# Kernel tuning notes

Measured on AMD Instinct MI355X. Metric: run time of the kernel, lower is better.

## Reference

```python
import jax, jax.numpy as jnp
import numpy as np

B, N, E = 8, 10000, 160000
D_IN, D_H = 128, 128
EPS = 1e-5


def setup_inputs() -> dict:
    key = jax.random.key(0)
    ks = jax.random.split(key, 10)
    x = jax.random.normal(ks[0], (B, N, D_IN), dtype=jnp.float32)
    h_prev = jax.random.normal(ks[1], (B, N, D_H), dtype=jnp.float32)
    edge_index = jax.random.randint(ks[2], (2, E), 0, N, dtype=jnp.int32)
    d_cat = D_IN + D_H
    s = 1.0 / np.sqrt(d_cat)
    def w(k):
        return jax.random.uniform(k, (d_cat, D_H), jnp.float32, -s, s)
    def b(k):
        return jax.random.uniform(k, (D_H,), jnp.float32, -s, s)
    return {
        "x": x, "edge_index": edge_index, "h_prev": h_prev,
        "Wz": w(ks[3]), "bz": b(ks[4]),
        "Wr": w(ks[5]), "br": b(ks[6]),
        "Wc": w(ks[7]), "bc": b(ks[8]),
        "gamma": jnp.ones((D_H,), jnp.float32),
        "beta": jnp.zeros((D_H,), jnp.float32),
    }


def _gcn(x, W, bias, src, dst, norm, n_nodes):
    # PyG GCNConv: linear transform, gather from src, weight by sym-norm, scatter-add to dst
    msg = (x @ W)[src] * norm[:, None]          # [E_total, D_H]
    return jax.ops.segment_sum(msg, dst, num_segments=n_nodes) + bias


def reference(x, edge_index, h_prev, Wz, bz, Wr, br, Wc, bc, gamma, beta):
    Bx, Nx, _ = x.shape
    BN = Bx * Nx
    x_flat = x.reshape(BN, -1)
    h_flat = h_prev.reshape(BN, -1)

    # batch the edge index with per-graph node offsets (all edges are in-range)
    offsets = (jnp.arange(Bx, dtype=edge_index.dtype) * Nx)[:, None]
    src = (edge_index[0][None, :] + offsets).reshape(-1)
    dst = (edge_index[1][None, :] + offsets).reshape(-1)

    # GCN self-loops + symmetric normalization (shared by all three convs)
    loops = jnp.arange(BN, dtype=src.dtype)
    src = jnp.concatenate([src, loops])
    dst = jnp.concatenate([dst, loops])
    deg = jax.ops.segment_sum(jnp.ones_like(dst, dtype=x.dtype), dst, num_segments=BN)
    dis = jnp.where(deg > 0, 1.0 / jnp.sqrt(jnp.maximum(deg, 1.0)), 0.0)
    norm = dis[src] * dis[dst]

    xh = jnp.concatenate([x_flat, h_flat], axis=1)
    z = jax.nn.sigmoid(_gcn(xh, Wz, bz, src, dst, norm, BN))
    r = jax.nn.sigmoid(_gcn(xh, Wr, br, src, dst, norm, BN))
    xrh = jnp.concatenate([x_flat, r * h_flat], axis=1)
    h_cand = jnp.tanh(_gcn(xrh, Wc, bc, src, dst, norm, BN))

    h_new = (1.0 - z) * h_flat + z * h_cand

    # LayerNorm over last dim
    mu = h_new.mean(axis=-1, keepdims=True)
    var = ((h_new - mu) ** 2).mean(axis=-1, keepdims=True)
    h_new = (h_new - mu) / jnp.sqrt(var + EPS) * gamma + beta
    return h_new.reshape(Bx, Nx, -1)
```

## Files before the change

kernel.cpp:

```cpp
#include <hip/hip_runtime.h>

#define NN 10000
#define BB 8
#define EE 160000
#define DH 128
#define LN_EPS 1e-5f

typedef unsigned short ushort_t;
typedef unsigned int uint_t;

typedef __bf16 bf16x8 __attribute__((ext_vector_type(8)));
typedef float floatx4 __attribute__((ext_vector_type(4)));
typedef float floatx2 __attribute__((ext_vector_type(2)));

__device__ __forceinline__ float b2f(uint_t u) { return __uint_as_float(u << 16); }
__device__ __forceinline__ ushort_t f2b(float f) {
    uint_t u = __float_as_uint(f);
    return (ushort_t)((u + 0x7fffu + ((u >> 16) & 1u)) >> 16);
}
__device__ __forceinline__ uint_t pack2(float lo, float hi) {
    return (uint_t)f2b(lo) | ((uint_t)f2b(hi) << 16);
}
__device__ __forceinline__ float sigm(float x) { return 1.0f / (1.0f + __expf(-x)); }
__device__ __forceinline__ float tanh_fast(float x) {
    float ex = __expf(2.0f * x);
    return 1.0f - 2.0f / (ex + 1.0f);
}

__device__ __forceinline__ floatx2 unpk(uint_t u) {
    floatx2 r;
    r.x = __uint_as_float(u << 16);
    r.y = __uint_as_float(u & 0xffff0000u);
    return r;
}
__device__ __forceinline__ void pk_fma(floatx2& a, floatx2 w, floatx2 v) {
    asm("v_pk_fma_f32 %0, %1, %2, %0" : "+v"(a) : "v"(w), "v"(v));
}
__device__ __forceinline__ void acc8p(floatx2* a, floatx2 w2, uint4 v) {
    pk_fma(a[0], w2, unpk(v.x));
    pk_fma(a[1], w2, unpk(v.y));
    pk_fma(a[2], w2, unpk(v.z));
    pk_fma(a[3], w2, unpk(v.w));
}


__global__ void count_deg(const int* __restrict__ ei, int* __restrict__ cnt) {
    int e = blockIdx.x * 256 + threadIdx.x;
    if (e < EE) atomicAdd(&cnt[ei[EE + e]], 1);
}

__global__ __launch_bounds__(256) void scan1(const int* __restrict__ cnt,
                                             int* __restrict__ offs,
                                             int* __restrict__ bsum) {
    __shared__ int s[256];
    const int t = threadIdx.x, idx = blockIdx.x * 256 + t;
    int x = (idx < NN) ? cnt[idx] : 0;
    s[t] = x;
    __syncthreads();
    for (int o = 1; o < 256; o <<= 1) {
        int v = s[t];
        int u = (t >= o) ? s[t - o] : 0;
        __syncthreads();
        s[t] = v + u;
        __syncthreads();
    }
    if (idx < NN) offs[idx] = s[t] - x;
    if (t == 255) bsum[blockIdx.x] = s[255];
}

__global__ __launch_bounds__(256) void scan3(const int* __restrict__ cnt,
                                             const int* __restrict__ bsum,
                                             int* __restrict__ offs,
                                             int* __restrict__ cursor,
                                             float* __restrict__ dis) {
    __shared__ int sb[40];
    __shared__ int pfx;
    const int t = threadIdx.x;
    if (t < 40) sb[t] = bsum[t];
    __syncthreads();
    if (t == 0) {
        int a = 0;
        for (int i = 0; i < blockIdx.x; ++i) a += sb[i];
        pfx = a;
    }
    __syncthreads();
    const int idx = blockIdx.x * 256 + t;
    if (idx < NN) {
        int off = offs[idx] + pfx;
        offs[idx] = off;
        cursor[idx] = off;
        dis[idx] = rsqrtf((float)(cnt[idx] + 1));
    }
    if (idx == 0) offs[NN] = EE;
}

__global__ void fill_csr(const int* __restrict__ ei, int* __restrict__ cursor,
                         const float* __restrict__ dis, int* __restrict__ csr_src,
                         ushort_t* __restrict__ csr_w) {
    int e = blockIdx.x * 256 + threadIdx.x;
    if (e < EE) {
        int s = ei[e];
        int d = ei[EE + e];
        int pos = atomicAdd(&cursor[d], 1);
        csr_src[pos] = s;
        csr_w[pos] = f2b(dis[s]);
    }
}


__global__ __launch_bounds__(256) void packwt_k(const float* __restrict__ x,
                                                const float* __restrict__ h,
                                                ushort_t* __restrict__ xb,
                                                ushort_t* __restrict__ hb,
                                                const float* __restrict__ Wz,
                                                const float* __restrict__ Wr,
                                                const float* __restrict__ Wc,
                                                ushort_t* __restrict__ Wt_zr,
                                                ushort_t* __restrict__ Wt_c) {
    if (blockIdx.x < 10000) {
        const size_t o = ((size_t)blockIdx.x * 256 + threadIdx.x) * 4;
        float4 vx = *(const float4*)(x + o);
        uint2 px;
        px.x = pack2(vx.x, vx.y);
        px.y = pack2(vx.z, vx.w);
        *(uint2*)(xb + o) = px;
        float4 vh = *(const float4*)(h + o);
        uint2 ph;
        ph.x = pack2(vh.x, vh.y);
        ph.y = pack2(vh.z, vh.w);
        *(uint2*)(hb + o) = ph;
    } else {
        const int col = blockIdx.x - 10000, k = threadIdx.x;
        if (col < 256) {
            float v = (col < 128) ? Wz[(size_t)k * 128 + col]
                                  : Wr[(size_t)k * 128 + col - 128];
            Wt_zr[(size_t)col * 256 + k] = f2b(v);
        } else {
            int c2 = col - 256;
            Wt_c[(size_t)c2 * 256 + k] = f2b(Wc[(size_t)k * 128 + c2]);
        }
    }
}


template <int NB>
__global__ __launch_bounds__(256) void gather4(
    const ushort_t* __restrict__ src0, const ushort_t* __restrict__ src1,
    const int* __restrict__ offs, const int* __restrict__ csr_src,
    const ushort_t* __restrict__ csr_w, const float* __restrict__ dis,
    ushort_t* __restrict__ dst0, ushort_t* __restrict__ dst1) {
    const int tid = threadIdx.x, lane = tid & 63;
    const int b = blockIdx.x & 7;
    const int n = (blockIdx.x >> 3) * 4 + (tid >> 6);
    const int g = lane >> 4, il = lane & 15;
    const ushort_t* base0 = src0 + (size_t)b * NN * 128;
    const ushort_t* base1 = (NB == 2) ? (src1 + (size_t)b * NN * 128) : base0;

    floatx2 a0[4], a1[4];
#pragma unroll
    for (int j = 0; j < 4; ++j) {
        a0[j] = (floatx2){0.f, 0.f};
        a1[j] = (floatx2){0.f, 0.f};
    }

    const float dn = dis[n];
    if (g == 0) {
        const floatx2 d2 = {dn, dn};
        const uint_t off = (uint_t)n * 128u + (uint_t)il * 8u;
        uint4 v = *(const uint4*)(base0 + off);
        acc8p(a0, d2, v);
        if (NB == 2) {
            uint4 vv = *(const uint4*)(base1 + off);
            acc8p(a1, d2, vv);
        }
    }

    const int e0 = offs[n], e1 = offs[n + 1];
    for (int ch = e0; ch < e1; ch += 64) {
        const int rem = e1 - ch;
        int idx = 0, wb = 0;
        if (lane < rem) {
            idx = csr_src[ch + lane];
            wb = (int)((uint_t)csr_w[ch + lane] << 16);
        }
        const int m = rem < 64 ? rem : 64;
        const int groups = (m + 3) >> 2;
        int pidx = g * 4;
#pragma unroll 4
        for (int i = 0; i < groups; ++i) {
            const int s = __builtin_amdgcn_ds_bpermute(pidx, idx);
            const float w =
                __uint_as_float((uint_t)__builtin_amdgcn_ds_bpermute(pidx, wb));
            pidx += 16;
            const floatx2 w2 = {w, w};
            const uint_t off = (uint_t)s * 128u + (uint_t)il * 8u;
            uint4 v = *(const uint4*)(base0 + off);
            acc8p(a0, w2, v);
            if (NB == 2) {
                uint4 vv = *(const uint4*)(base1 + off);
                acc8p(a1, w2, vv);
            }
        }
    }

    float o0[8], o1[8];
#pragma unroll
    for (int j = 0; j < 4; ++j) {
        o0[2 * j] = a0[j].x;
        o0[2 * j + 1] = a0[j].y;
        o1[2 * j] = a1[j].x;
        o1[2 * j + 1] = a1[j].y;
    }
#pragma unroll
    for (int j = 0; j < 8; ++j) {
        o0[j] *= dn;
        o0[j] += __shfl_xor(o0[j], 16);
        o0[j] += __shfl_xor(o0[j], 32);
    }
    if (NB == 2) {
#pragma unroll
        for (int j = 0; j < 8; ++j) {
            o1[j] *= dn;
            o1[j] += __shfl_xor(o1[j], 16);
            o1[j] += __shfl_xor(o1[j], 32);
        }
    }

    if (lane < 16) {
        const size_t o = ((size_t)b * NN + n) * 128 + (size_t)il * 8;
        uint4 st;
        st.x = pack2(o0[0], o0[1]);
        st.y = pack2(o0[2], o0[3]);
        st.z = pack2(o0[4], o0[5]);
        st.w = pack2(o0[6], o0[7]);
        *(uint4*)(dst0 + o) = st;
        if (NB == 2) {
            uint4 st1;
            st1.x = pack2(o1[0], o1[1]);
            st1.y = pack2(o1[2], o1[3]);
            st1.z = pack2(o1[4], o1[5]);
            st1.w = pack2(o1[6], o1[7]);
            *(uint4*)(dst1 + o) = st1;
        }
    }
}


template <int PHASE>
__global__ __launch_bounds__(512) void gemm_k(
    const ushort_t* __restrict__ A1, const ushort_t* __restrict__ A2,
    const ushort_t* __restrict__ Wt, const float* __restrict__ bz,
    const float* __restrict__ br, const float* __restrict__ bc,
    const float* __restrict__ h_prev, const ushort_t* __restrict__ z_in,
    const float* __restrict__ gamma, const float* __restrict__ beta,
    ushort_t* __restrict__ z_out, ushort_t* __restrict__ rh_out,
    float* __restrict__ f_out) {
    __shared__ __align__(16) ushort_t As[128 * 72];
    __shared__ __align__(16) ushort_t Bs[128 * 72];
    const int tid = threadIdx.x;
    const int rb0 = blockIdx.x * 128;
    const int mode = (PHASE == 1) ? 2 : blockIdx.y;
    const int cb0 = (mode == 1) ? 128 : 0;

    const int wv = tid >> 6, lane = tid & 63;
    const int l15 = lane & 15, q = lane >> 4;
    const int sr = tid >> 2;
    const int kh = (tid & 3) * 16;

    floatx4 acc[8];
#pragma unroll
    for (int j = 0; j < 8; ++j) acc[j] = (floatx4){0.f, 0.f, 0.f, 0.f};

    uint4 pa0, pa1, pb0, pb1;
#define LOAD_AB(k0)                                                                   \
    {                                                                                 \
        const int kg = (k0) + kh;                                                     \
        const ushort_t* sA = (kg < 128)                                               \
                                 ? (A1 + (size_t)(rb0 + sr) * 128 + kg)               \
                                 : (A2 + (size_t)(rb0 + sr) * 128 + (kg - 128));      \
        pa0 = *(const uint4*)(sA);                                                    \
        pa1 = *(const uint4*)(sA + 8);                                                \
        const ushort_t* sB = Wt + (size_t)(cb0 + sr) * 256 + (k0) + kh;               \
        pb0 = *(const uint4*)(sB);                                                    \
        pb1 = *(const uint4*)(sB + 8);                                                \
    }

    LOAD_AB(0);
#pragma unroll
    for (int t = 0; t < 4; ++t) {
        if (t) __syncthreads();
        *(uint4*)(&As[sr * 72 + kh]) = pa0;
        *(uint4*)(&As[sr * 72 + kh + 8]) = pa1;
        *(uint4*)(&Bs[sr * 72 + kh]) = pb0;
        *(uint4*)(&Bs[sr * 72 + kh + 8]) = pb1;
        __syncthreads();
        if (t < 3) LOAD_AB((t + 1) * 64);
#pragma unroll
        for (int ks = 0; ks < 2; ++ks) {
            const int ko = ks * 32 + q * 8;
            bf16x8 a0 = *(const bf16x8*)&As[(wv * 16 + l15) * 72 + ko];
#pragma unroll
            for (int j = 0; j < 8; ++j) {
                bf16x8 b = *(const bf16x8*)&Bs[(j * 16 + l15) * 72 + ko];
                acc[j] = __builtin_amdgcn_mfma_f32_16x16x32_bf16(a0, b, acc[j], 0, 0, 0);
            }
        }
    }
#undef LOAD_AB

    if (mode == 0) {
        float bv[8];
#pragma unroll
        for (int j = 0; j < 8; ++j) bv[j] = bz[j * 16 + l15];
#pragma unroll
        for (int j = 0; j < 8; ++j)
#pragma unroll
            for (int v = 0; v < 4; ++v) {
                int row = rb0 + wv * 16 + q * 4 + v;
                z_out[(size_t)row * 128 + j * 16 + l15] = f2b(sigm(acc[j][v] + bv[j]));
            }
    } else if (mode == 1) {
        float bv[8];
#pragma unroll
        for (int j = 0; j < 8; ++j) bv[j] = br[j * 16 + l15];
#pragma unroll
        for (int j = 0; j < 8; ++j)
#pragma unroll
            for (int v = 0; v < 4; ++v) {
                int row = rb0 + wv * 16 + q * 4 + v;
                float r = sigm(acc[j][v] + bv[j]);
                float hh = h_prev[(size_t)row * 128 + j * 16 + l15];
                rh_out[(size_t)row * 128 + j * 16 + l15] = f2b(r * hh);
            }
    } else {
        float bv[8], gv[8], bev[8];
#pragma unroll
        for (int j = 0; j < 8; ++j) {
            bv[j] = bc[j * 16 + l15];
            gv[j] = gamma[j * 16 + l15];
            bev[j] = beta[j * 16 + l15];
        }
#pragma unroll
        for (int v = 0; v < 4; ++v) {
            const int row = rb0 + wv * 16 + q * 4 + v;
            float hn[8];
            float s = 0.f;
#pragma unroll
            for (int j = 0; j < 8; ++j) {
                float hc = tanh_fast(acc[j][v] + bv[j]);
                float zz = b2f((uint_t)z_in[(size_t)row * 128 + j * 16 + l15]);
                float hh = h_prev[(size_t)row * 128 + j * 16 + l15];
                hn[j] = (1.0f - zz) * hh + zz * hc;
                s += hn[j];
            }
#pragma unroll
            for (int o = 8; o > 0; o >>= 1) s += __shfl_xor(s, o);
            float mu = s * (1.0f / 128.0f);
            float vv = 0.f;
#pragma unroll
            for (int j = 0; j < 8; ++j) {
                float d = hn[j] - mu;
                vv += d * d;
            }
#pragma unroll
            for (int o = 8; o > 0; o >>= 1) vv += __shfl_xor(vv, o);
            float inv = rsqrtf(vv * (1.0f / 128.0f) + LN_EPS);
#pragma unroll
            for (int j = 0; j < 8; ++j)
                f_out[(size_t)row * 128 + j * 16 + l15] =
                    (hn[j] - mu) * inv * gv[j] + bev[j];
        }
    }
}


extern "C" void kernel_launch(void* const* d_in, const int* in_sizes, int n_in,
                              void* d_out, int out_size, void* d_ws, size_t ws_size,
                              hipStream_t stream) {
    const float* x = (const float*)d_in[0];
    const int* ei = (const int*)d_in[1];
    const float* h = (const float*)d_in[2];
    const float* Wz = (const float*)d_in[3];
    const float* bz = (const float*)d_in[4];
    const float* Wr = (const float*)d_in[5];
    const float* br = (const float*)d_in[6];
    const float* Wc = (const float*)d_in[7];
    const float* bcv = (const float*)d_in[8];
    const float* gamma = (const float*)d_in[9];
    const float* beta = (const float*)d_in[10];
    float* out = (float*)d_out;

    char* w = (char*)d_ws;
    int* offs = (int*)(w + 0);
    float* dis = (float*)(w + 40960);
    int* csr_src = (int*)(w + 81920);
    ushort_t* csr_w = (ushort_t*)(w + 721920);
    ushort_t* Wt_zr = (ushort_t*)(w + 1041920);
    ushort_t* Wt_c = (ushort_t*)(w + 1172992);
    ushort_t* xb = (ushort_t*)(w + 1239040);
    ushort_t* hb = (ushort_t*)(w + 21719040);
    ushort_t* agg_x = (ushort_t*)(w + 42199040);
    ushort_t* agg_h = (ushort_t*)(w + 62679040);
    int* cnt = (int*)(w + 1239040);
    int* cursor = (int*)(w + 1280000);
    int* bsum = (int*)(w + 1320000);
    ushort_t* z_buf = xb;
    ushort_t* rh_bf = hb;
    ushort_t* agg_rh = agg_h;

    hipMemsetAsync(cnt, 0, NN * sizeof(int), stream);
    count_deg<<<EE / 256, 256, 0, stream>>>(ei, cnt);
    scan1<<<40, 256, 0, stream>>>(cnt, offs, bsum);
    scan3<<<40, 256, 0, stream>>>(cnt, bsum, offs, cursor, dis);
    fill_csr<<<EE / 256, 256, 0, stream>>>(ei, cursor, dis, csr_src, csr_w);
    packwt_k<<<10384, 256, 0, stream>>>(x, h, xb, hb, Wz, Wr, Wc, Wt_zr, Wt_c);

    gather4<2><<<(BB * NN) / 4, 256, 0, stream>>>(xb, hb, offs, csr_src, csr_w, dis,
                                                  agg_x, agg_h);
    gemm_k<0><<<dim3(80000 / 128, 2), 512, 0, stream>>>(
        agg_x, agg_h, Wt_zr, bz, br, bcv, h, (const ushort_t*)0, gamma, beta,
        z_buf, rh_bf, (float*)0);
    gather4<1><<<(BB * NN) / 4, 256, 0, stream>>>(rh_bf, (const ushort_t*)0, offs,
                                                  csr_src, csr_w, dis, agg_rh,
                                                  (ushort_t*)0);
    gemm_k<1><<<dim3(80000 / 128, 1), 512, 0, stream>>>(
        agg_x, agg_rh, Wt_c, bz, br, bcv, h, z_buf, gamma, beta,
        (ushort_t*)0, (ushort_t*)0, out);
}
```

Measured before the change: 316.7 us.

## Assign one node per 16-lane group in gather instead of one per wavefront

The gather kernel now processes four destination nodes per wavefront, one per 16-lane group, instead of spreading a single node's edges across four groups. This removes the cross-group shuffle reduction at the end, and every lane now stores its result. The launch covers 16 nodes per block. The cost is divergence: each wave loops to the maximum degree among its four nodes and masks off idle groups, so skewed degrees waste some work.

```diff
diff --git a/kernel.cpp b/kernel.cpp
--- a/kernel.cpp
+++ b/kernel.cpp
@@ -144,17 +144,18 @@
 
 
 template <int NB>
-__global__ __launch_bounds__(256) void gather4(
+__global__ __launch_bounds__(256) void gather16(
     const ushort_t* __restrict__ src0, const ushort_t* __restrict__ src1,
     const int* __restrict__ offs, const int* __restrict__ csr_src,
     const ushort_t* __restrict__ csr_w, const float* __restrict__ dis,
     ushort_t* __restrict__ dst0, ushort_t* __restrict__ dst1) {
     const int tid = threadIdx.x, lane = tid & 63;
     const int b = blockIdx.x & 7;
-    const int n = (blockIdx.x >> 3) * 4 + (tid >> 6);
     const int g = lane >> 4, il = lane & 15;
+    const int ng = (blockIdx.x >> 3) * 16 + (tid >> 6) * 4 + g;
     const ushort_t* base0 = src0 + (size_t)b * NN * 128;
     const ushort_t* base1 = (NB == 2) ? (src1 + (size_t)b * NN * 128) : base0;
+    const uint_t cofs = (uint_t)il * 8u;
 
     floatx2 a0[4], a1[4];
 #pragma unroll
@@ -163,85 +164,61 @@
         a1[j] = (floatx2){0.f, 0.f};
     }
 
-    const float dn = dis[n];
-    if (g == 0) {
+    const int e0 = offs[ng], e1 = offs[ng + 1];
+    const int deg = e1 - e0;
+    const float dn = dis[ng];
+
+    {
         const floatx2 d2 = {dn, dn};
-        const uint_t off = (uint_t)n * 128u + (uint_t)il * 8u;
-        uint4 v = *(const uint4*)(base0 + off);
-        acc8p(a0, d2, v);
-        if (NB == 2) {
-            uint4 vv = *(const uint4*)(base1 + off);
-            acc8p(a1, d2, vv);
-        }
-    }
-
-    const int e0 = offs[n], e1 = offs[n + 1];
-    for (int ch = e0; ch < e1; ch += 64) {
-        const int rem = e1 - ch;
+        const uint_t off = (uint_t)ng * 128u + cofs;
+        acc8p(a0, d2, *(const uint4*)(base0 + off));
+        if (NB == 2) acc8p(a1, d2, *(const uint4*)(base1 + off));
+    }
+
+    int mx = deg;
+    mx = max(mx, __shfl_xor(mx, 16));
+    mx = max(mx, __shfl_xor(mx, 32));
+    const int dmax = __builtin_amdgcn_readfirstlane(mx);
+    const int pbase = (lane & 48) << 2;
+
+    for (int ibase = 0; ibase < dmax; ibase += 16) {
         int idx = 0, wb = 0;
-        if (lane < rem) {
-            idx = csr_src[ch + lane];
-            wb = (int)((uint_t)csr_w[ch + lane] << 16);
-        }
-        const int m = rem < 64 ? rem : 64;
-        const int groups = (m + 3) >> 2;
-        int pidx = g * 4;
+        const int pos = e0 + ibase + il;
+        if (pos < e1) {
+            idx = csr_src[pos];
+            wb = (int)((uint_t)csr_w[pos] << 16);
+        }
+        const int lim = (dmax - ibase) < 16 ? (dmax - ibase) : 16;
+        int pidx = pbase;
 #pragma unroll 4
-        for (int i = 0; i < groups; ++i) {
+        for (int i = 0; i < lim; ++i) {
             const int s = __builtin_amdgcn_ds_bpermute(pidx, idx);
-            const float w =
+            const float wgt =
                 __uint_as_float((uint_t)__builtin_amdgcn_ds_bpermute(pidx, wb));
-            pidx += 16;
-            const floatx2 w2 = {w, w};
-            const uint_t off = (uint_t)s * 128u + (uint_t)il * 8u;
-            uint4 v = *(const uint4*)(base0 + off);
-            acc8p(a0, w2, v);
-            if (NB == 2) {
-                uint4 vv = *(const uint4*)(base1 + off);
-                acc8p(a1, w2, vv);
-            }
-        }
-    }
-
-    float o0[8], o1[8];
-#pragma unroll
-    for (int j = 0; j < 4; ++j) {
-        o0[2 * j] = a0[j].x;
-        o0[2 * j + 1] = a0[j].y;
-        o1[2 * j] = a1[j].x;
-        o1[2 * j + 1] = a1[j].y;
-    }
-#pragma unroll
-    for (int j = 0; j < 8; ++j) {
-        o0[j] *= dn;
-        o0[j] += __shfl_xor(o0[j], 16);
-        o0[j] += __shfl_xor(o0[j], 32);
-    }
+            pidx += 4;
+            if (ibase + i < deg) {
+                const floatx2 w2 = {wgt, wgt};
+                const uint_t off = (uint_t)s * 128u + cofs;
+                acc8p(a0, w2, *(const uint4*)(base0 + off));
+                if (NB == 2) acc8p(a1, w2, *(const uint4*)(base1 + off));
+            }
+        }
+    }
+
+    const size_t o = ((size_t)b * NN + ng) * 128 + cofs;
+    uint4 st;
+    st.x = pack2(a0[0].x * dn, a0[0].y * dn);
+    st.y = pack2(a0[1].x * dn, a0[1].y * dn);
+    st.z = pack2(a0[2].x * dn, a0[2].y * dn);
+    st.w = pack2(a0[3].x * dn, a0[3].y * dn);
+    *(uint4*)(dst0 + o) = st;
     if (NB == 2) {
-#pragma unroll
-        for (int j = 0; j < 8; ++j) {
-            o1[j] *= dn;
-            o1[j] += __shfl_xor(o1[j], 16);
-            o1[j] += __shfl_xor(o1[j], 32);
-        }
-    }
-
-    if (lane < 16) {
-        const size_t o = ((size_t)b * NN + n) * 128 + (size_t)il * 8;
-        uint4 st;
-        st.x = pack2(o0[0], o0[1]);
-        st.y = pack2(o0[2], o0[3]);
-        st.z = pack2(o0[4], o0[5]);
-        st.w = pack2(o0[6], o0[7]);
-        *(uint4*)(dst0 + o) = st;
-        if (NB == 2) {
-            uint4 st1;
-            st1.x = pack2(o1[0], o1[1]);
-            st1.y = pack2(o1[2], o1[3]);
-            st1.z = pack2(o1[4], o1[5]);
-            st1.w = pack2(o1[6], o1[7]);
-            *(uint4*)(dst1 + o) = st1;
-        }
+        uint4 st1;
+        st1.x = pack2(a1[0].x * dn, a1[0].y * dn);
+        st1.y = pack2(a1[1].x * dn, a1[1].y * dn);
+        st1.z = pack2(a1[2].x * dn, a1[2].y * dn);
+        st1.w = pack2(a1[3].x * dn, a1[3].y * dn);
+        *(uint4*)(dst1 + o) = st1;
     }
 }
 
@@ -415,14 +392,14 @@
     fill_csr<<<EE / 256, 256, 0, stream>>>(ei, cursor, dis, csr_src, csr_w);
     packwt_k<<<10384, 256, 0, stream>>>(x, h, xb, hb, Wz, Wr, Wc, Wt_zr, Wt_c);
 
-    gather4<2><<<(BB * NN) / 4, 256, 0, stream>>>(xb, hb, offs, csr_src, csr_w, dis,
-                                                  agg_x, agg_h);
+    gather16<2><<<(NN / 16) * 8, 256, 0, stream>>>(xb, hb, offs, csr_src, csr_w, dis,
+                                                   agg_x, agg_h);
     gemm_k<0><<<dim3(80000 / 128, 2), 512, 0, stream>>>(
         agg_x, agg_h, Wt_zr, bz, br, bcv, h, (const ushort_t*)0, gamma, beta,
         z_buf, rh_bf, (float*)0);
-    gather4<1><<<(BB * NN) / 4, 256, 0, stream>>>(rh_bf, (const ushort_t*)0, offs,
-                                                  csr_src, csr_w, dis, agg_rh,
-                                                  (ushort_t*)0);
+    gather16<1><<<(NN / 16) * 8, 256, 0, stream>>>(rh_bf, (const ushort_t*)0, offs,
+                                                   csr_src, csr_w, dis, agg_rh,
+                                                   (ushort_t*)0);
     gemm_k<1><<<dim3(80000 / 128, 1), 512, 0, stream>>>(
         agg_x, agg_rh, Wt_c, bz, br, bcv, h, z_buf, gamma, beta,
         (ushort_t*)0, (ushort_t*)0, out);
```

Result: faster. 302.5 us (-4.5%).
